# Kernel tuning notes

Hardware: AMD Instinct MI355X
Metric: run time of the kernel (lower is better)

## Reference

```python
import math
import jax, jax.numpy as jnp
import numpy as np

B, L, D_M, H, D_K, D_V = 2, 2048, 1024, 16, 64, 64


def setup_inputs() -> dict:
    key = jax.random.key(0)
    ks = jax.random.split(key, 12)
    s_in = 1.0 / math.sqrt(D_M)
    s_cat = 1.0 / math.sqrt(H * D_V)
    return {
        "Q": jax.random.normal(ks[0], (B, L, D_M), jnp.float32),
        "K": jax.random.normal(ks[1], (B, L, D_M), jnp.float32),
        "V": jax.random.normal(ks[2], (B, L, D_M), jnp.float32),
        # per-head projections batched along a leading head axis
        "Wq": jax.random.uniform(ks[3], (H, D_M, D_K), jnp.float32, -s_in, s_in),
        "bq": jax.random.uniform(ks[4], (H, D_K), jnp.float32, -s_in, s_in),
        "Wk": jax.random.uniform(ks[5], (H, D_M, D_K), jnp.float32, -s_in, s_in),
        "bk": jax.random.uniform(ks[6], (H, D_K), jnp.float32, -s_in, s_in),
        "Wv": jax.random.uniform(ks[7], (H, D_M, D_V), jnp.float32, -s_in, s_in),
        "bv": jax.random.uniform(ks[8], (H, D_V), jnp.float32, -s_in, s_in),
        "Wo": jax.random.uniform(ks[9], (H * D_V, D_M), jnp.float32, -s_cat, s_cat),
        "bo": jax.random.uniform(ks[10], (D_M,), jnp.float32, -s_cat, s_cat),
    }


def reference(Q, K, V, Wq, bq, Wk, bk, Wv, bv, Wo, bo):
    # Batched per-head projections: [B,L,Dm] x [H,Dm,Dk] -> [B,H,L,Dk]
    Qp = jnp.einsum("bqm,hmk->bhqk", Q, Wq) + bq[None, :, None, :]
    Kp = jnp.einsum("bsm,hmk->bhsk", K, Wk) + bk[None, :, None, :]
    Vp = jnp.einsum("bsm,hmv->bhsv", V, Wv) + bv[None, :, None, :]
    scores = jnp.einsum("bhqk,bhsk->bhqs", Qp, Kp) / jnp.sqrt(
        jnp.asarray(D_K, Qp.dtype)
    )
    # NOTE: original torch code uses Softmax(dim=1) on a [B,Lq,Lk] matrix,
    # i.e. normalization over the QUERY axis (axis=2 here), not the key axis.
    attn = jax.nn.softmax(scores, axis=2)
    wV = jnp.einsum("bhqs,bhsv->bhqv", attn, Vp)  # [B,H,Lq,Dv]
    cat_V = jnp.transpose(wV, (0, 2, 1, 3)).reshape(B, L, H * D_V)
    return cat_V @ Wo + bo
```

## Files before the change

### kernel.cpp

```cpp
#include <hip/hip_runtime.h>
#include <hip/hip_bf16.h>

#define DEVI __device__ __forceinline__

typedef __hip_bfloat16 bf16;
typedef __attribute__((ext_vector_type(8))) __bf16 bf16x8;
typedef __attribute__((ext_vector_type(4))) float f32x4;
typedef __attribute__((ext_vector_type(16))) float f32x16;
typedef __attribute__((ext_vector_type(4))) short short4v;
typedef __attribute__((ext_vector_type(8))) short short8v;


DEVI short bfbits(float f) { bf16 h = __float2bfloat16(f); return *(short*)&h; }
DEVI float b2f(short s) { union { float f; unsigned u; } c; c.u = ((unsigned)(unsigned short)s) << 16; return c.f; }

DEVI void gl16(const void* g, void* l) {
  __builtin_amdgcn_global_load_lds((const __attribute__((address_space(1))) void*)g,
                                   (__attribute__((address_space(3))) void*)l, 16, 0, 0);
}

DEVI f32x4 MF(bf16x8 a, bf16x8 b, f32x4 c) {
  return __builtin_amdgcn_mfma_f32_16x16x32_bf16(a, b, c, 0, 0, 0);
}
DEVI f32x16 MF32(bf16x8 a, bf16x8 b, f32x16 c) {
  return __builtin_amdgcn_mfma_f32_32x32x16_bf16(a, b, c, 0, 0, 0);
}

DEVI unsigned cvtpk(float lo, float hi) {
  unsigned w;
  asm("v_cvt_pk_bf16_f32 %0, %1, %2" : "=v"(w) : "v"(lo), "v"(hi));
  return w;
}
DEVI void swap32(unsigned& a, unsigned& b) {
  asm volatile("v_permlane32_swap_b32 %0, %1" : "+v"(a), "+v"(b));
}
DEVI bf16x8 packB(unsigned w0, unsigned w1, unsigned w2, unsigned w3) {
  union { unsigned u[4]; bf16x8 v; } t;
  t.u[0] = w0; t.u[1] = w1; t.u[2] = w2; t.u[3] = w3;
  return t.v;
}

DEVI int swzE(int row, int ec) { return row * 64 + (ec ^ ((row & 7) << 3)); }
DEVI int srcC(int boff) { return (boff & 127) ^ (((boff >> 7) & 7) << 4); }

__global__ __launch_bounds__(256) void k_cvt_qkv(
    const float* __restrict__ Q, const float* __restrict__ K, const float* __restrict__ V,
    bf16* __restrict__ Qb, bf16* __restrict__ Kb, bf16* __restrict__ Vb) {
  const float* s = blockIdx.y == 0 ? Q : (blockIdx.y == 1 ? K : V);
  bf16* d = blockIdx.y == 0 ? Qb : (blockIdx.y == 1 ? Kb : Vb);
  int i = (blockIdx.x * 256 + threadIdx.x) * 4;
  float4 v = *(const float4*)(s + i);
  short4v o;
  o[0] = bfbits(v.x); o[1] = bfbits(v.y); o[2] = bfbits(v.z); o[3] = bfbits(v.w);
  *(short4v*)(d + i) = o;
}

__global__ __launch_bounds__(256) void k_prep_w(
    const float* __restrict__ Wq, const float* __restrict__ Wk, const float* __restrict__ Wv,
    const float* __restrict__ Wo,
    bf16* __restrict__ WqT, bf16* __restrict__ WkT, bf16* __restrict__ WvT,
    bf16* __restrict__ WoT) {
  __shared__ float t[64][65];
  const int z = blockIdx.z;
  const float* in; bf16* out; int ldin, ldout;
  if (z < 3) {
    const float* W = z == 0 ? Wq : (z == 1 ? Wk : Wv);
    bf16* O = z == 0 ? WqT : (z == 1 ? WkT : WvT);
    const int hh = blockIdx.y, m0 = blockIdx.x * 64;
    in = W + hh * 65536 + m0 * 64; ldin = 64;
    out = O + hh * 65536 + m0;     ldout = 1024;
  } else {
    const int r0 = blockIdx.x * 64, c0 = blockIdx.y * 64;
    in = Wo + r0 * 1024 + c0; ldin = 1024;
    out = WoT + c0 * 1024 + r0; ldout = 1024;
  }
  const int tx = threadIdx.x & 63, ty = threadIdx.x >> 6;
  for (int r = ty; r < 64; r += 4) t[r][tx] = in[r * ldin + tx];
  __syncthreads();
  for (int c = ty; c < 64; c += 4) out[c * ldout + tx] = __float2bfloat16(t[tx][c]);
}

__global__ __launch_bounds__(256) void k_proj_gemm(
    const bf16* __restrict__ Qb, const bf16* __restrict__ Kb, const bf16* __restrict__ Vb,
    const bf16* __restrict__ WqT, const bf16* __restrict__ WkT, const bf16* __restrict__ WvT,
    const float* __restrict__ bq, const float* __restrict__ bk, const float* __restrict__ bv,
    bf16* __restrict__ Qp, bf16* __restrict__ Kp, bf16* __restrict__ VpT) {
  __shared__ bf16 smem[17408];
  bf16* As = smem;
  bf16* Bs = smem + 8192;
  const int z = blockIdx.z;
  const bf16* A  = z == 0 ? Qb : (z == 1 ? Kb : Vb);
  const bf16* BT = z == 0 ? WqT : (z == 1 ? WkT : WvT);
  const float* bias = z == 0 ? bq : (z == 1 ? bk : bv);
  const int row0 = blockIdx.x * 128, col0 = blockIdx.y * 128;
  const int tid = threadIdx.x, lane = tid & 63, wave = tid >> 6;
  const int wq = wave >> 1, wn = wave & 1;
  f32x4 acc[4][4];
#pragma unroll
  for (int i = 0; i < 4; ++i)
#pragma unroll
    for (int j = 0; j < 4; ++j) acc[i][j] = (f32x4)0.0f;

  for (int k0 = 0; k0 < 1024; k0 += 64) {
#pragma unroll
    for (int it = 0; it < 4; ++it) {
      int boff = (it * 4 + wave) * 1024 + lane * 16;
      int r = boff >> 7, c = srcC(boff);
      gl16((const char*)A  + (size_t)(row0 + r) * 2048 + k0 * 2 + c, (char*)As + boff);
      gl16((const char*)BT + (size_t)(col0 + r) * 2048 + k0 * 2 + c, (char*)Bs + boff);
    }
    __syncthreads();
#pragma unroll
    for (int ks = 0; ks < 2; ++ks) {
      bf16x8 a[4], b[4];
#pragma unroll
      for (int i = 0; i < 4; ++i)
        a[i] = *(const bf16x8*)&As[swzE(wq * 64 + i * 16 + (lane & 15), ks * 32 + (lane >> 4) * 8)];
#pragma unroll
      for (int j = 0; j < 4; ++j)
        b[j] = *(const bf16x8*)&Bs[swzE(wn * 64 + j * 16 + (lane & 15), ks * 32 + (lane >> 4) * 8)];
#pragma unroll
      for (int i = 0; i < 4; ++i)
#pragma unroll
        for (int j = 0; j < 4; ++j) acc[i][j] = MF(a[i], b[j], acc[i][j]);
    }
    __syncthreads();
  }

  if (z < 2) {
    const float scl = (z == 0) ? 0.125f : 1.0f;
    bf16* C = z == 0 ? Qp : Kp;
#pragma unroll
    for (int i = 0; i < 4; ++i)
#pragma unroll
      for (int j = 0; j < 4; ++j) {
        int col = col0 + wn * 64 + j * 16 + (lane & 15);
        float bb = bias[col];
#pragma unroll
        for (int r = 0; r < 4; ++r) {
          int row = row0 + wq * 64 + i * 16 + (lane >> 4) * 4 + r;
          C[row * 1024 + col] = __float2bfloat16((acc[i][j][r] + bb) * scl);
        }
      }
  } else {
    bf16* T = smem;
#pragma unroll
    for (int i = 0; i < 4; ++i)
#pragma unroll
      for (int j = 0; j < 4; ++j) {
        int nl = wn * 64 + j * 16 + (lane & 15);
        float bb = bias[col0 + nl];
#pragma unroll
        for (int r = 0; r < 4; ++r) {
          int sl = wq * 64 + i * 16 + (lane >> 4) * 4 + r;
          T[nl * 136 + sl] = __float2bfloat16(acc[i][j][r] + bb);
        }
      }
    __syncthreads();
    const int b = row0 >> 11, lr = row0 & 2047;
    const int nl = tid >> 1, half = tid & 1;
    const int n = col0 + nl;
    bf16* drow = VpT + ((size_t)(b * 16 + (n >> 6)) * 64 + (n & 63)) * 2048 + lr + half * 64;
#pragma unroll
    for (int k = 0; k < 8; ++k)
      *(short8v*)(drow + k * 8) = *(const short8v*)&T[nl * 136 + half * 64 + k * 8];
  }
}

__global__ __launch_bounds__(256, 2) void k_stats(
    const bf16* __restrict__ Qp, const bf16* __restrict__ Kp, bf16* __restrict__ VpT) {
  __shared__ bf16 Kband[128 * 64];
  __shared__ bf16 Qs[2][64 * 64];
  __shared__ float zs[128];
  const int id = blockIdx.x;
  const int sw = (id & 7) * 64 + (id >> 3);
  const int bh = sw >> 4, s0 = (sw & 15) * 128;
  const int b = bh >> 4, h = bh & 15;
  const char* Qrow = (const char*)(Qp + (size_t)(b * 2048) * 1024 + h * 64);
  const char* Krow = (const char*)(Kp + (size_t)(b * 2048) * 1024 + h * 64);
  const int tid = threadIdx.x, lane = tid & 63, wq = tid >> 6;
  const int ln31 = lane & 31, hf = lane >> 5;

  {
    int boff = tid * 16;
#pragma unroll
    for (int it = 0; it < 4; ++it) {
      int bo = boff + it * 4096;
      gl16(Krow + (size_t)(s0 + (bo >> 7)) * 2048 + srcC(bo), (char*)Kband + bo);
    }
    gl16(Qrow + (size_t)(boff >> 7) * 2048 + srcC(boff), (char*)Qs[0] + boff);
    gl16(Qrow + (size_t)((boff + 4096) >> 7) * 2048 + srcC(boff + 4096), (char*)Qs[0] + boff + 4096);
  }
  __syncthreads();
  bf16x8 kf[4];
#pragma unroll
  for (int ks = 0; ks < 4; ++ks)
    kf[ks] = *(const bf16x8*)&Kband[swzE(wq * 32 + ln31, ks * 16 + hf * 8)];

  float zp[16];
#pragma unroll
  for (int r = 0; r < 16; ++r) zp[r] = 0.f;

  for (int c = 0; c < 32; ++c) {
    const int p = c & 1;
    if (c < 31) {
      int boff = tid * 16;
      gl16(Qrow + (size_t)((c + 1) * 64 + (boff >> 7)) * 2048 + srcC(boff), (char*)Qs[p ^ 1] + boff);
      gl16(Qrow + (size_t)((c + 1) * 64 + ((boff + 4096) >> 7)) * 2048 + srcC(boff + 4096),
           (char*)Qs[p ^ 1] + boff + 4096);
    }
    f32x16 sacc0 = (f32x16)0.0f, sacc1 = (f32x16)0.0f;
#pragma unroll
    for (int ks = 0; ks < 4; ++ks) {
      bf16x8 qf0 = *(const bf16x8*)&Qs[p][swzE(ln31, ks * 16 + hf * 8)];
      bf16x8 qf1 = *(const bf16x8*)&Qs[p][swzE(32 + ln31, ks * 16 + hf * 8)];
      sacc0 = MF32(kf[ks], qf0, sacc0);
      sacc1 = MF32(kf[ks], qf1, sacc1);
    }
#pragma unroll
    for (int r = 0; r < 16; ++r) zp[r] += __expf(sacc0[r]) + __expf(sacc1[r]);
    __syncthreads();
  }
#pragma unroll
  for (int m = 1; m <= 16; m <<= 1)
#pragma unroll
    for (int r = 0; r < 16; ++r) zp[r] += __shfl_xor(zp[r], m);
  if (ln31 == 0) {
#pragma unroll
    for (int r = 0; r < 16; ++r)
      zs[wq * 32 + (r & 3) + 8 * (r >> 2) + 4 * hf] = 1.0f / zp[r];
  }
  __syncthreads();
  {
    const int v = tid >> 2, sseg = (tid & 3) * 32;
    bf16* base = VpT + (size_t)(bh * 64 + v) * 2048 + s0 + sseg;
#pragma unroll
    for (int t = 0; t < 4; ++t) {
      short8v x = *(const short8v*)(base + t * 8);
      short8v o;
#pragma unroll
      for (int j = 0; j < 8; ++j) o[j] = bfbits(b2f(x[j]) * zs[sseg + t * 8 + j]);
      *(short8v*)(base + t * 8) = o;
    }
  }
}

__global__ __launch_bounds__(256, 2) void k_attn_pv(
    const bf16* __restrict__ Qp, const bf16* __restrict__ Kp, const bf16* __restrict__ VpT,
    bf16* __restrict__ wV) {
  __shared__ bf16 Qs[128 * 64];
  __shared__ bf16 Ks[2][64 * 64];
  __shared__ bf16 Vs[2][64 * 64];
  const int id = blockIdx.x;
  const int sw = (id & 7) * 64 + (id >> 3);
  const int bh = sw >> 4, q0 = (sw & 15) * 128;
  const int b = bh >> 4, h = bh & 15;
  const char* Qrow = (const char*)(Qp + (size_t)(b * 2048) * 1024 + h * 64);
  const char* Krow = (const char*)(Kp + (size_t)(b * 2048) * 1024 + h * 64);
  const char* Vrow = (const char*)(VpT + (size_t)bh * 64 * 2048);
  const int tid = threadIdx.x, lane = tid & 63, wq = tid >> 6;
  const int ln31 = lane & 31, hf = lane >> 5;

  {
    int boff = tid * 16;
#pragma unroll
    for (int it = 0; it < 4; ++it) {
      int bo = boff + it * 4096;
      gl16(Qrow + (size_t)(q0 + (bo >> 7)) * 2048 + srcC(bo), (char*)Qs + bo);
    }
#pragma unroll
    for (int it = 0; it < 2; ++it) {
      int bo = boff + it * 4096;
      gl16(Krow + (size_t)(bo >> 7) * 2048 + srcC(bo), (char*)Ks[0] + bo);
      gl16(Vrow + (size_t)(bo >> 7) * 4096 + srcC(bo), (char*)Vs[0] + bo);
    }
  }
  __syncthreads();
  bf16x8 qf[4];
#pragma unroll
  for (int ks = 0; ks < 4; ++ks)
    qf[ks] = *(const bf16x8*)&Qs[swzE(wq * 32 + ln31, ks * 16 + hf * 8)];

  f32x16 oacc0 = (f32x16)0.0f, oacc1 = (f32x16)0.0f;

  for (int c = 0; c < 32; ++c) {
    const int p = c & 1;
    if (c < 31) {
      int boff = tid * 16;
#pragma unroll
      for (int it = 0; it < 2; ++it) {
        int bo = boff + it * 4096;
        gl16(Krow + (size_t)((c + 1) * 64 + (bo >> 7)) * 2048 + srcC(bo), (char*)Ks[p ^ 1] + bo);
        gl16(Vrow + (size_t)(bo >> 7) * 4096 + (c + 1) * 128 + srcC(bo), (char*)Vs[p ^ 1] + bo);
      }
    }
    f32x16 sacc0 = (f32x16)0.0f, sacc1 = (f32x16)0.0f;
#pragma unroll
    for (int ks = 0; ks < 4; ++ks) {
      bf16x8 kf0 = *(const bf16x8*)&Ks[p][swzE(ln31, ks * 16 + hf * 8)];
      bf16x8 kf1 = *(const bf16x8*)&Ks[p][swzE(32 + ln31, ks * 16 + hf * 8)];
      sacc0 = MF32(kf0, qf[ks], sacc0);
      sacc1 = MF32(kf1, qf[ks], sacc1);
    }
    bf16x8 bfr[4];
#pragma unroll
    for (int sb = 0; sb < 2; ++sb) {
      const f32x16& sa = sb ? sacc1 : sacc0;
      float pz[16];
#pragma unroll
      for (int r = 0; r < 16; ++r) pz[r] = __expf(sa[r]);
#pragma unroll
      for (int half = 0; half < 2; ++half) {
        unsigned w0 = cvtpk(pz[half * 8 + 0], pz[half * 8 + 1]);
        unsigned w2 = cvtpk(pz[half * 8 + 4], pz[half * 8 + 5]);
        unsigned w1 = cvtpk(pz[half * 8 + 2], pz[half * 8 + 3]);
        unsigned w3 = cvtpk(pz[half * 8 + 6], pz[half * 8 + 7]);
        swap32(w0, w2);
        swap32(w1, w3);
        bfr[sb * 2 + half] = packB(w0, w1, w2, w3);
      }
    }
#pragma unroll
    for (int ks = 0; ks < 4; ++ks) {
      bf16x8 vf0 = *(const bf16x8*)&Vs[p][swzE(ln31, ks * 16 + hf * 8)];
      bf16x8 vf1 = *(const bf16x8*)&Vs[p][swzE(32 + ln31, ks * 16 + hf * 8)];
      oacc0 = MF32(vf0, bfr[ks], oacc0);
      oacc1 = MF32(vf1, bfr[ks], oacc1);
    }
    __syncthreads();
  }

  {
    char* row = (char*)(wV + ((size_t)bh * 2048 + q0 + wq * 32 + ln31) * 64);
#pragma unroll
    for (int vb = 0; vb < 2; ++vb) {
      const f32x16& oa = vb ? oacc1 : oacc0;
#pragma unroll
      for (int qd = 0; qd < 4; ++qd) {
        uint2 w;
        w.x = cvtpk(oa[qd * 4 + 0], oa[qd * 4 + 1]);
        w.y = cvtpk(oa[qd * 4 + 2], oa[qd * 4 + 3]);
        *(uint2*)(row + vb * 64 + qd * 16 + hf * 8) = w;
      }
    }
  }
}

__global__ __launch_bounds__(256) void k_out_gemm(
    const bf16* __restrict__ wV, const bf16* __restrict__ WoT, const float* __restrict__ bo,
    float* __restrict__ out) {
  __shared__ bf16 As[128 * 64], Bs[128 * 64];
  const int row0 = blockIdx.x * 128, col0 = blockIdx.y * 128;
  const int tid = threadIdx.x, lane = tid & 63, wave = tid >> 6;
  const int wq = wave >> 1, wn = wave & 1;
  const int b = row0 >> 11, lr = row0 & 2047;
  f32x4 acc[4][4];
#pragma unroll
  for (int i = 0; i < 4; ++i)
#pragma unroll
    for (int j = 0; j < 4; ++j) acc[i][j] = (f32x4)0.0f;

  for (int k0 = 0; k0 < 1024; k0 += 64) {
    const char* Abase = (const char*)(wV + ((size_t)(b * 16 + (k0 >> 6)) * 2048 + lr) * 64);
#pragma unroll
    for (int it = 0; it < 4; ++it) {
      int boff = (it * 4 + wave) * 1024 + lane * 16;
      int r = boff >> 7, c = srcC(boff);
      gl16(Abase + (size_t)r * 128 + c, (char*)As + boff);
      gl16((const char*)WoT + (size_t)(col0 + r) * 2048 + k0 * 2 + c, (char*)Bs + boff);
    }
    __syncthreads();
#pragma unroll
    for (int ks = 0; ks < 2; ++ks) {
      bf16x8 a[4], bb[4];
#pragma unroll
      for (int i = 0; i < 4; ++i)
        a[i] = *(const bf16x8*)&As[swzE(wq * 64 + i * 16 + (lane & 15), ks * 32 + (lane >> 4) * 8)];
#pragma unroll
      for (int j = 0; j < 4; ++j)
        bb[j] = *(const bf16x8*)&Bs[swzE(wn * 64 + j * 16 + (lane & 15), ks * 32 + (lane >> 4) * 8)];
#pragma unroll
      for (int i = 0; i < 4; ++i)
#pragma unroll
        for (int j = 0; j < 4; ++j) acc[i][j] = MF(a[i], bb[j], acc[i][j]);
    }
    __syncthreads();
  }
#pragma unroll
  for (int i = 0; i < 4; ++i)
#pragma unroll
    for (int j = 0; j < 4; ++j) {
      int col = col0 + wn * 64 + j * 16 + (lane & 15);
      float bb = bo[col];
#pragma unroll
      for (int r = 0; r < 4; ++r) {
        int row = row0 + wq * 64 + i * 16 + (lane >> 4) * 4 + r;
        out[row * 1024 + col] = acc[i][j][r] + bb;
      }
    }
}

extern "C" void kernel_launch(void* const* d_in, const int* in_sizes, int n_in,
                              void* d_out, int out_size, void* d_ws, size_t ws_size,
                              hipStream_t stream) {
  (void)in_sizes; (void)n_in; (void)out_size; (void)ws_size;
  const float* Q  = (const float*)d_in[0];
  const float* K  = (const float*)d_in[1];
  const float* V  = (const float*)d_in[2];
  const float* Wq = (const float*)d_in[3];
  const float* bq = (const float*)d_in[4];
  const float* Wk = (const float*)d_in[5];
  const float* bk = (const float*)d_in[6];
  const float* Wv = (const float*)d_in[7];
  const float* bv = (const float*)d_in[8];
  const float* Wo = (const float*)d_in[9];
  const float* bo = (const float*)d_in[10];

  char* ws = (char*)d_ws;
  bf16* Qb  = (bf16*)(ws);
  bf16* Kb  = (bf16*)(ws + (8u  << 20));
  bf16* Vb  = (bf16*)(ws + (16u << 20));
  bf16* WqT = (bf16*)(ws + (24u << 20));
  bf16* WkT = (bf16*)(ws + (26u << 20));
  bf16* WvT = (bf16*)(ws + (28u << 20));
  bf16* WoT = (bf16*)(ws + (30u << 20));
  bf16* Qp  = (bf16*)(ws + (32u << 20));
  bf16* Kp  = (bf16*)(ws + (40u << 20));
  bf16* VpT = (bf16*)(ws + (48u << 20));
  bf16* wVn = (bf16*)(ws + (56u << 20));

  k_cvt_qkv <<<dim3(4096, 3), 256, 0, stream>>>(Q, K, V, Qb, Kb, Vb);
  k_prep_w  <<<dim3(16, 16, 4), 256, 0, stream>>>(Wq, Wk, Wv, Wo, WqT, WkT, WvT, WoT);
  k_proj_gemm<<<dim3(32, 8, 3), 256, 0, stream>>>(Qb, Kb, Vb, WqT, WkT, WvT, bq, bk, bv, Qp, Kp, VpT);
  k_stats   <<<512, 256, 0, stream>>>(Qp, Kp, VpT);
  k_attn_pv <<<512, 256, 0, stream>>>(Qp, Kp, VpT, wVn);
  k_out_gemm<<<dim3(32, 8), 256, 0, stream>>>(wVn, WoT, bo, (float*)d_out);
}
```

Before: 261.5 us.

## Triple-buffer Q and K/V tiles with explicit vmcnt waits in attention kernels

Moves the k_stats and k_attn_pv loops from double to triple buffering. Tiles are prefetched two iterations ahead, and the blanket __syncthreads is replaced by explicit s_waitcnt vmcnt counts, raw s_barrier and scheduling barriers. The goal is to hide global-to-LDS load latency better and avoid draining all outstanding loads every iteration. LDS use grows by 8 KB in k_stats and 16 KB in k_attn_pv, which may reduce occupancy. The hand-counted vmcnt values must match the number of loads issued.

```diff
diff --git a/kernel.cpp b/kernel.cpp
--- a/kernel.cpp
+++ b/kernel.cpp
@@ -39,6 +39,10 @@
   t.u[0] = w0; t.u[1] = w1; t.u[2] = w2; t.u[3] = w3;
   return t.v;
 }
+
+#define WAITV(N) asm volatile("s_waitcnt vmcnt(" #N ")" ::: "memory")
+#define SBAR __builtin_amdgcn_s_barrier()
+#define SCHED0 __builtin_amdgcn_sched_barrier(0)
 
 DEVI int swzE(int row, int ec) { return row * 64 + (ec ^ ((row & 7) << 3)); }
 DEVI int srcC(int boff) { return (boff & 127) ^ (((boff >> 7) & 7) << 4); }
@@ -170,7 +174,7 @@
 __global__ __launch_bounds__(256, 2) void k_stats(
     const bf16* __restrict__ Qp, const bf16* __restrict__ Kp, bf16* __restrict__ VpT) {
   __shared__ bf16 Kband[128 * 64];
-  __shared__ bf16 Qs[2][64 * 64];
+  __shared__ bf16 Qs[3][64 * 64];
   __shared__ float zs[128];
   const int id = blockIdx.x;
   const int sw = (id & 7) * 64 + (id >> 3);
@@ -180,18 +184,20 @@
   const char* Krow = (const char*)(Kp + (size_t)(b * 2048) * 1024 + h * 64);
   const int tid = threadIdx.x, lane = tid & 63, wq = tid >> 6;
   const int ln31 = lane & 31, hf = lane >> 5;
-
-  {
-    int boff = tid * 16;
-#pragma unroll
-    for (int it = 0; it < 4; ++it) {
-      int bo = boff + it * 4096;
-      gl16(Krow + (size_t)(s0 + (bo >> 7)) * 2048 + srcC(bo), (char*)Kband + bo);
-    }
-    gl16(Qrow + (size_t)(boff >> 7) * 2048 + srcC(boff), (char*)Qs[0] + boff);
-    gl16(Qrow + (size_t)((boff + 4096) >> 7) * 2048 + srcC(boff + 4096), (char*)Qs[0] + boff + 4096);
-  }
-  __syncthreads();
+  const int boff = tid * 16;
+
+#pragma unroll
+  for (int it = 0; it < 4; ++it) {
+    int bo = boff + it * 4096;
+    gl16(Krow + (size_t)(s0 + (bo >> 7)) * 2048 + srcC(bo), (char*)Kband + bo);
+  }
+#pragma unroll
+  for (int cc = 0; cc < 3; ++cc) {
+    gl16(Qrow + (size_t)(cc * 64 + (boff >> 7)) * 2048 + srcC(boff), (char*)Qs[cc] + boff);
+    gl16(Qrow + (size_t)(cc * 64 + ((boff + 4096) >> 7)) * 2048 + srcC(boff + 4096),
+         (char*)Qs[cc] + boff + 4096);
+  }
+  WAITV(6); SBAR; SCHED0;
   bf16x8 kf[4];
 #pragma unroll
   for (int ks = 0; ks < 4; ++ks)
@@ -202,13 +208,9 @@
   for (int r = 0; r < 16; ++r) zp[r] = 0.f;
 
   for (int c = 0; c < 32; ++c) {
-    const int p = c & 1;
-    if (c < 31) {
-      int boff = tid * 16;
-      gl16(Qrow + (size_t)((c + 1) * 64 + (boff >> 7)) * 2048 + srcC(boff), (char*)Qs[p ^ 1] + boff);
-      gl16(Qrow + (size_t)((c + 1) * 64 + ((boff + 4096) >> 7)) * 2048 + srcC(boff + 4096),
-           (char*)Qs[p ^ 1] + boff + 4096);
-    }
+    const int p = c % 3;
+    if (c <= 29) { WAITV(4); } else if (c == 30) { WAITV(2); } else { WAITV(0); }
+    SBAR; SCHED0;
     f32x16 sacc0 = (f32x16)0.0f, sacc1 = (f32x16)0.0f;
 #pragma unroll
     for (int ks = 0; ks < 4; ++ks) {
@@ -219,7 +221,12 @@
     }
 #pragma unroll
     for (int r = 0; r < 16; ++r) zp[r] += __expf(sacc0[r]) + __expf(sacc1[r]);
-    __syncthreads();
+    SCHED0; SBAR;
+    if (c < 29) {
+      gl16(Qrow + (size_t)((c + 3) * 64 + (boff >> 7)) * 2048 + srcC(boff), (char*)Qs[p] + boff);
+      gl16(Qrow + (size_t)((c + 3) * 64 + ((boff + 4096) >> 7)) * 2048 + srcC(boff + 4096),
+           (char*)Qs[p] + boff + 4096);
+    }
   }
 #pragma unroll
   for (int m = 1; m <= 16; m <<= 1)
@@ -249,8 +256,8 @@
     const bf16* __restrict__ Qp, const bf16* __restrict__ Kp, const bf16* __restrict__ VpT,
     bf16* __restrict__ wV) {
   __shared__ bf16 Qs[128 * 64];
-  __shared__ bf16 Ks[2][64 * 64];
-  __shared__ bf16 Vs[2][64 * 64];
+  __shared__ bf16 Ks[3][64 * 64];
+  __shared__ bf16 Vs[3][64 * 64];
   const int id = blockIdx.x;
   const int sw = (id & 7) * 64 + (id >> 3);
   const int bh = sw >> 4, q0 = (sw & 15) * 128;
@@ -260,22 +267,23 @@
   const char* Vrow = (const char*)(VpT + (size_t)bh * 64 * 2048);
   const int tid = threadIdx.x, lane = tid & 63, wq = tid >> 6;
   const int ln31 = lane & 31, hf = lane >> 5;
-
-  {
-    int boff = tid * 16;
-#pragma unroll
-    for (int it = 0; it < 4; ++it) {
-      int bo = boff + it * 4096;
-      gl16(Qrow + (size_t)(q0 + (bo >> 7)) * 2048 + srcC(bo), (char*)Qs + bo);
-    }
+  const int boff = tid * 16;
+
+#pragma unroll
+  for (int it = 0; it < 4; ++it) {
+    int bo = boff + it * 4096;
+    gl16(Qrow + (size_t)(q0 + (bo >> 7)) * 2048 + srcC(bo), (char*)Qs + bo);
+  }
+#pragma unroll
+  for (int cc = 0; cc < 3; ++cc) {
 #pragma unroll
     for (int it = 0; it < 2; ++it) {
       int bo = boff + it * 4096;
-      gl16(Krow + (size_t)(bo >> 7) * 2048 + srcC(bo), (char*)Ks[0] + bo);
-      gl16(Vrow + (size_t)(bo >> 7) * 4096 + srcC(bo), (char*)Vs[0] + bo);
-    }
-  }
-  __syncthreads();
+      gl16(Krow + (size_t)(cc * 64 + (bo >> 7)) * 2048 + srcC(bo), (char*)Ks[cc] + bo);
+      gl16(Vrow + (size_t)(bo >> 7) * 4096 + cc * 128 + srcC(bo), (char*)Vs[cc] + bo);
+    }
+  }
+  WAITV(12); SBAR; SCHED0;
   bf16x8 qf[4];
 #pragma unroll
   for (int ks = 0; ks < 4; ++ks)
@@ -284,16 +292,9 @@
   f32x16 oacc0 = (f32x16)0.0f, oacc1 = (f32x16)0.0f;
 
   for (int c = 0; c < 32; ++c) {
-    const int p = c & 1;
-    if (c < 31) {
-      int boff = tid * 16;
-#pragma unroll
-      for (int it = 0; it < 2; ++it) {
-        int bo = boff + it * 4096;
-        gl16(Krow + (size_t)((c + 1) * 64 + (bo >> 7)) * 2048 + srcC(bo), (char*)Ks[p ^ 1] + bo);
-        gl16(Vrow + (size_t)(bo >> 7) * 4096 + (c + 1) * 128 + srcC(bo), (char*)Vs[p ^ 1] + bo);
-      }
-    }
+    const int p = c % 3;
+    if (c <= 29) { WAITV(8); } else if (c == 30) { WAITV(4); } else { WAITV(0); }
+    SBAR; SCHED0;
     f32x16 sacc0 = (f32x16)0.0f, sacc1 = (f32x16)0.0f;
 #pragma unroll
     for (int ks = 0; ks < 4; ++ks) {
@@ -327,7 +328,15 @@
       oacc0 = MF32(vf0, bfr[ks], oacc0);
       oacc1 = MF32(vf1, bfr[ks], oacc1);
     }
-    __syncthreads();
+    SCHED0; SBAR;
+    if (c < 29) {
+#pragma unroll
+      for (int it = 0; it < 2; ++it) {
+        int bo = boff + it * 4096;
+        gl16(Krow + (size_t)((c + 3) * 64 + (bo >> 7)) * 2048 + srcC(bo), (char*)Ks[p] + bo);
+        gl16(Vrow + (size_t)(bo >> 7) * 4096 + (c + 3) * 128 + srcC(bo), (char*)Vs[p] + bo);
+      }
+    }
   }
 
   {
```

Result: no change. 258.9 us (-1.0%).
